# Kernel optimization log

Hardware: AMD Instinct MI355X
Metric: run time of the kernel (lower is better)

The kernel has to match this reference:

```python
import jax, jax.numpy as jnp
import numpy as np

BH = 32  # block_h
BW = 32  # block_w
M, K, N = 4096, 4096, 4096  # tokens, in_features, out_features


def setup_inputs() -> dict:
    key = jax.random.key(0)
    k1, k2, k3, k4 = jax.random.split(key, 4)
    data = jax.random.normal(k1, (M, K), dtype=jnp.float32)
    weight = jax.random.normal(k2, (N, K), dtype=jnp.float32) * 0.02
    bias = jax.random.normal(k3, (N,), dtype=jnp.float32) * 0.02
    # elementwise 0/1 mask over the weight matrix
    mask = jax.random.randint(k4, (N, K), 0, 2, dtype=jnp.int32)
    # conv bias of the 1x1-channel block-summing conv; chosen so ~half the
    # 32x32 blocks (sum ~ Binomial(1024, 0.5)) end up inactive
    conv_bias = jnp.full((1,), -512.0, dtype=jnp.float32)
    return {"data": data, "weight": weight, "bias": bias, "mask": mask,
            "conv_bias": conv_bias}


def reference(data, weight, bias, mask, conv_bias):
    n_out, n_in = weight.shape
    nH, nW = n_out // BH, n_in // BW
    # conv2d with all-ones (BH,BW) kernel, stride (BH,BW) == per-block sum + bias
    block_sum = mask.astype(jnp.float32).reshape(nH, BH, nW, BW).sum(axis=(1, 3))
    block_mask = (block_sum + conv_bias[0]) > 0  # [nH, nW] bool
    # dds matmul (trans_b=True): zero inactive weight blocks, out = data @ W^T
    w_blocks = weight.reshape(nH, BH, nW, BW)
    w_masked = (w_blocks * block_mask[:, None, :, None].astype(weight.dtype)
                ).reshape(n_out, n_in)
    out = jnp.einsum('mk,nk->mn', data, w_masked) + bias
    return out
```

## Files before the change

### kernel.cpp

```cpp
#include <hip/hip_runtime.h>
#include <hip/hip_bf16.h>
#include <stdint.h>

#define M_DIM 4096
#define N_DIM 4096
#define K_DIM 4096
#define NH 128
#define NW 128
#define NKT 64

typedef short bf16x8 __attribute__((ext_vector_type(8)));
typedef short bf16x4 __attribute__((ext_vector_type(4)));
typedef float f32x4 __attribute__((ext_vector_type(4)));

#define MFMA(a, b, c) __builtin_amdgcn_mfma_f32_16x16x32_bf16((a), (b), (c), 0, 0, 0)

__device__ __forceinline__ short f2bf(float f) {
  union { float f; unsigned u; } c; c.f = f;
  unsigned u = c.u;
  unsigned r = (u + 0x7fffu + ((u >> 16) & 1u)) >> 16;
  return (short)r;
}

__global__ __launch_bounds__(256) void k_block_mask(const int* __restrict__ mask,
                                                    const float* __restrict__ conv_bias,
                                                    int* __restrict__ bm) {
  const int bw = blockIdx.x, bh = blockIdx.y;
  const int t = threadIdx.x;
  const int row = t >> 3;
  const int c4 = (t & 7) << 2;
  const int4* p = (const int4*)(mask + (size_t)(bh * 32 + row) * K_DIM + bw * 32 + c4);
  int4 v = *p;
  int s = v.x + v.y + v.z + v.w;
#pragma unroll
  for (int off = 32; off > 0; off >>= 1) s += __shfl_down(s, off);
  __shared__ int red[4];
  if ((t & 63) == 0) red[t >> 6] = s;
  __syncthreads();
  if (t == 0) {
    float tot = (float)(red[0] + red[1] + red[2] + red[3]) + conv_bias[0];
    bm[bh * NW + bw] = (tot > 0.0f) ? 1 : 0;
  }
}

__global__ __launch_bounds__(256) void k_cvt_data(const float* __restrict__ in,
                                                  short* __restrict__ ob) {
  size_t i = (size_t)blockIdx.x * 256 + threadIdx.x;
  f32x4 v = ((const f32x4*)in)[i];
  bf16x4 o;
  o[0] = f2bf(v[0]); o[1] = f2bf(v[1]); o[2] = f2bf(v[2]); o[3] = f2bf(v[3]);
  ((bf16x4*)ob)[i] = o;
}

__global__ __launch_bounds__(256) void k_cvt_weight(const float* __restrict__ w,
                                                    const int* __restrict__ bm,
                                                    short* __restrict__ ob) {
  size_t i = (size_t)blockIdx.x * 256 + threadIdx.x;
  int n = (int)(i >> 10);
  int k = ((int)i & 1023) << 2;
  float m = bm[((n >> 5) << 7) + (k >> 5)] ? 1.0f : 0.0f;
  f32x4 v = ((const f32x4*)w)[i];
  bf16x4 o;
  o[0] = f2bf(v[0] * m); o[1] = f2bf(v[1] * m);
  o[2] = f2bf(v[2] * m); o[3] = f2bf(v[3] * m);
  ((bf16x4*)ob)[i] = o;
}

__global__ __launch_bounds__(512, 2) void k_gemm256(const short* __restrict__ Ab,
                                                    const short* __restrict__ Bb,
                                                    const float* __restrict__ bias,
                                                    const int* __restrict__ bm,
                                                    float* __restrict__ out) {
  __shared__ short Asm[2][2][256][32];
  __shared__ short Bsm[2][2][256][32];

  const int tid = threadIdx.x;
  const int wid = tid >> 6, lane = tid & 63;
  const int r = lane & 15, g0 = lane >> 4;
  const int gs = g0 ^ ((r >> 1) & 3);

  const int swz = (blockIdx.x & 7) * 32 + (blockIdx.x >> 3);
  const int bx = swz & 15, by = swz >> 4;
  const int rowM = by * 256, colN = bx * 256;

  const int srow = tid >> 2;
  const int sseg = (tid & 3) ^ ((tid >> 3) & 3);
  const int swave = wid * 512;

  const short* gA = Ab + (size_t)(rowM + srow) * K_DIM + sseg * 8;
  const short* gB = Bb + (size_t)(colN + srow) * K_DIM + sseg * 8;
  const size_t HOFF = (size_t)128 * K_DIM;

  const int* bp = bm + (size_t)(colN >> 5) * NW;
  unsigned long long m0l = __ballot(bp[0 * 128 + lane] != 0);
  unsigned long long m0h = __ballot(bp[0 * 128 + 64 + lane] != 0);
  unsigned long long m1l = __ballot(bp[1 * 128 + lane] != 0);
  unsigned long long m1h = __ballot(bp[1 * 128 + 64 + lane] != 0);
  unsigned long long m2l = __ballot(bp[2 * 128 + lane] != 0);
  unsigned long long m2h = __ballot(bp[2 * 128 + 64 + lane] != 0);
  unsigned long long m3l = __ballot(bp[3 * 128 + lane] != 0);
  unsigned long long m3h = __ballot(bp[3 * 128 + 64 + lane] != 0);
  unsigned long long m4l = __ballot(bp[4 * 128 + lane] != 0);
  unsigned long long m4h = __ballot(bp[4 * 128 + 64 + lane] != 0);
  unsigned long long m5l = __ballot(bp[5 * 128 + lane] != 0);
  unsigned long long m5h = __ballot(bp[5 * 128 + 64 + lane] != 0);
  unsigned long long m6l = __ballot(bp[6 * 128 + lane] != 0);
  unsigned long long m6h = __ballot(bp[6 * 128 + 64 + lane] != 0);
  unsigned long long m7l = __ballot(bp[7 * 128 + lane] != 0);
  unsigned long long m7h = __ballot(bp[7 * 128 + 64 + lane] != 0);
  __builtin_amdgcn_sched_barrier(0);

#define BTJ(J, kc) ((int)((((kc) & 64) ? m##J##h : m##J##l) >> ((kc) & 63)) & 1)

#define GLL(g, l)                                                            \
  __builtin_amdgcn_global_load_lds((const __attribute__((address_space(1))) void*)(g), \
                                   (__attribute__((address_space(3))) void*)(l), 16, 0, 0)
#define STA(BUF, kt, h, ks) GLL(gA + HOFF * (h) + (size_t)(kt) * 64 + (ks) * 32, \
                                &Asm[BUF][ks][(h) * 128][0] + swave)
#define STB(BUF, kt, h, ks) GLL(gB + HOFF * (h) + (size_t)(kt) * 64 + (ks) * 32, \
                                &Bsm[BUF][ks][(h) * 128][0] + swave)

#define LDA(BUF, ks, m) (*(const bf16x8*)&Asm[BUF][ks][wid * 32 + (m) * 16 + r][gs * 8])
#define LDB(BUF, ks, n) (*(const bf16x8*)&Bsm[BUF][ks][(n) * 16 + r][gs * 8])

#define MFJ(A0, A1, B0, B1, f)                                               \
  acc[0][f] = MFMA(A0, B0, acc[0][f]);   acc[1][f] = MFMA(A1, B0, acc[1][f]); \
  acc[0][(f) + 1] = MFMA(A0, B1, acc[0][(f) + 1]);                           \
  acc[1][(f) + 1] = MFMA(A1, B1, acc[1][(f) + 1]);

#define BAR __builtin_amdgcn_s_barrier()
#define SB0 __builtin_amdgcn_sched_barrier(0)
#define PRIO1 __builtin_amdgcn_s_setprio(1)
#define PRIO0 __builtin_amdgcn_s_setprio(0)
#define VMW_(N) asm volatile("s_waitcnt vmcnt(" #N ")" ::: "memory")
#define VMW(N) VMW_(N)

#define TILE(BUF, NB, u, SB, SA, SR, VM0, VM2)                               \
  {                                                                          \
    const int kb = 2 * (u);                                                  \
    const int c0 = BTJ(0, kb), c1 = BTJ(1, kb), c2 = BTJ(2, kb), c3 = BTJ(3, kb); \
    const int c4 = BTJ(4, kb), c5 = BTJ(5, kb), c6 = BTJ(6, kb), c7 = BTJ(7, kb); \
    const int d0 = BTJ(0, kb + 1), d1 = BTJ(1, kb + 1), d2 = BTJ(2, kb + 1), d3 = BTJ(3, kb + 1); \
    const int d4 = BTJ(4, kb + 1), d5 = BTJ(5, kb + 1), d6 = BTJ(6, kb + 1), d7 = BTJ(7, kb + 1); \
                  \
    BAR; SB0;                                                                \
    aY0 = LDA(BUF, 1, 0); aY1 = LDA(BUF, 1, 1);                              \
    if (c4) { bB[0] = LDB(BUF, 0, 8);  bB[1] = LDB(BUF, 0, 9); }             \
    if (c5) { bB[2] = LDB(BUF, 0, 10); bB[3] = LDB(BUF, 0, 11); }            \
    if (c6) { bB[4] = LDB(BUF, 0, 12); bB[5] = LDB(BUF, 0, 13); }            \
    if (c7) { bB[6] = LDB(BUF, 0, 14); bB[7] = LDB(BUF, 0, 15); }            \
    PRIO1;                                                                   \
    if (c0) { MFJ(aX0, aX1, bA[0], bA[1], 0) }                               \
    if (c1) { MFJ(aX0, aX1, bA[2], bA[3], 2) }                               \
    if (c2) { MFJ(aX0, aX1, bA[4], bA[5], 4) }                               \
    if (c3) { MFJ(aX0, aX1, bA[6], bA[7], 6) }                               \
    PRIO0;                                                                   \
    if (SB) { STB(NB, (u) + 1, 0, 0); STB(NB, (u) + 1, 1, 0); }              \
    VMW(VM0);                                                                \
                          \
    BAR; SB0;                                                                \
    if (d0) { bA[0] = LDB(BUF, 1, 0); bA[1] = LDB(BUF, 1, 1); }              \
    if (d1) { bA[2] = LDB(BUF, 1, 2); bA[3] = LDB(BUF, 1, 3); }              \
    if (d2) { bA[4] = LDB(BUF, 1, 4); bA[5] = LDB(BUF, 1, 5); }              \
    if (d3) { bA[6] = LDB(BUF, 1, 6); bA[7] = LDB(BUF, 1, 7); }              \
    PRIO1;                                                                   \
    if (c4) { MFJ(aX0, aX1, bB[0], bB[1], 8) }                               \
    if (c5) { MFJ(aX0, aX1, bB[2], bB[3], 10) }                              \
    if (c6) { MFJ(aX0, aX1, bB[4], bB[5], 12) }                              \
    if (c7) { MFJ(aX0, aX1, bB[6], bB[7], 14) }                              \
    PRIO0;                                                                   \
    if (SB) { STB(NB, (u) + 1, 0, 1); STB(NB, (u) + 1, 1, 1); }              \
                          \
    BAR; SB0;                                                                \
    if (d4) { bB[0] = LDB(BUF, 1, 8);  bB[1] = LDB(BUF, 1, 9); }             \
    if (d5) { bB[2] = LDB(BUF, 1, 10); bB[3] = LDB(BUF, 1, 11); }            \
    if (d6) { bB[4] = LDB(BUF, 1, 12); bB[5] = LDB(BUF, 1, 13); }            \
    if (d7) { bB[6] = LDB(BUF, 1, 14); bB[7] = LDB(BUF, 1, 15); }            \
    PRIO1;                                                                   \
    if (d0) { MFJ(aY0, aY1, bA[0], bA[1], 0) }                               \
    if (d1) { MFJ(aY0, aY1, bA[2], bA[3], 2) }                               \
    if (d2) { MFJ(aY0, aY1, bA[4], bA[5], 4) }                               \
    if (d3) { MFJ(aY0, aY1, bA[6], bA[7], 6) }                               \
    PRIO0;                                                                   \
    if (SA) { STA(BUF, (u) + 2, 0, 0); STA(BUF, (u) + 2, 1, 0); }            \
    VMW(VM2);                                                                \
       \
    BAR; SB0;                                                                \
    if (SR) {                                                                \
      const int n0 = BTJ(0, kb + 2), n1 = BTJ(1, kb + 2);                    \
      const int n2 = BTJ(2, kb + 2), n3 = BTJ(3, kb + 2);                    \
      aX0 = LDA(NB, 0, 0); aX1 = LDA(NB, 0, 1);                              \
      if (n0) { bA[0] = LDB(NB, 0, 0); bA[1] = LDB(NB, 0, 1); }              \
      if (n1) { bA[2] = LDB(NB, 0, 2); bA[3] = LDB(NB, 0, 3); }              \
      if (n2) { bA[4] = LDB(NB, 0, 4); bA[5] = LDB(NB, 0, 5); }              \
      if (n3) { bA[6] = LDB(NB, 0, 6); bA[7] = LDB(NB, 0, 7); }              \
    }                                                                        \
    PRIO1;                                                                   \
    if (d4) { MFJ(aY0, aY1, bB[0], bB[1], 8) }                               \
    if (d5) { MFJ(aY0, aY1, bB[2], bB[3], 10) }                              \
    if (d6) { MFJ(aY0, aY1, bB[4], bB[5], 12) }                              \
    if (d7) { MFJ(aY0, aY1, bB[6], bB[7], 14) }                              \
    PRIO0;                                                                   \
    if (SA) { STA(BUF, (u) + 2, 0, 1); STA(BUF, (u) + 2, 1, 1); }            \
  }

  f32x4 acc[2][16];
#pragma unroll
  for (int m = 0; m < 2; ++m)
#pragma unroll
    for (int n = 0; n < 16; ++n) acc[m][n] = (f32x4){0.f, 0.f, 0.f, 0.f};

  bf16x8 aX0, aX1, aY0, aY1, bA[8], bB[8];

  STA(0, 0, 0, 0); STA(0, 0, 1, 0); STA(0, 0, 0, 1); STA(0, 0, 1, 1);
  STB(0, 0, 0, 0); STB(0, 0, 1, 0); STB(0, 0, 0, 1); STB(0, 0, 1, 1);
  STA(1, 1, 0, 0); STA(1, 1, 1, 0); STA(1, 1, 0, 1); STA(1, 1, 1, 1);
  VMW(4);
  BAR; SB0;
  {
    const int p0 = BTJ(0, 0), p1 = BTJ(1, 0), p2 = BTJ(2, 0), p3 = BTJ(3, 0);
    aX0 = LDA(0, 0, 0); aX1 = LDA(0, 0, 1);
    if (p0) { bA[0] = LDB(0, 0, 0); bA[1] = LDB(0, 0, 1); }
    if (p1) { bA[2] = LDB(0, 0, 2); bA[3] = LDB(0, 0, 3); }
    if (p2) { bA[4] = LDB(0, 0, 4); bA[5] = LDB(0, 0, 5); }
    if (p3) { bA[6] = LDB(0, 0, 6); bA[7] = LDB(0, 0, 7); }
  }

#pragma unroll 1
  for (int u = 0; u < NKT - 2; u += 2) {
    TILE(0, 1, u, 1, 1, 1, 6, 4);
    TILE(1, 0, u + 1, 1, 1, 1, 6, 4);
  }
  TILE(0, 1, NKT - 2, 1, 0, 1, 6, 2);
  TILE(1, 0, NKT - 1, 0, 0, 0, 0, 0);

  const int orow = rowM + wid * 32;
#pragma unroll
  for (int n = 0; n < 16; ++n) {
    int col = colN + n * 16 + r;
    float bz = bias[col];
#pragma unroll
    for (int m = 0; m < 2; ++m) {
      int row0 = orow + m * 16 + g0 * 4;
#pragma unroll
      for (int j = 0; j < 4; ++j)
        out[(size_t)(row0 + j) * N_DIM + col] = acc[m][n][j] + bz;
    }
  }
#undef TILE
#undef GLL
#undef STA
#undef STB
#undef LDA
#undef LDB
#undef MFJ
#undef BAR
#undef SB0
#undef PRIO1
#undef PRIO0
#undef VMW
#undef VMW_
#undef BTJ
}

__global__ __launch_bounds__(256) void k_naive(const float* __restrict__ A,
                                               const float* __restrict__ W,
                                               const float* __restrict__ bias,
                                               const int* __restrict__ bm,
                                               float* __restrict__ out) {
  int col = blockIdx.x * 16 + (threadIdx.x & 15);
  int row = blockIdx.y * 16 + (threadIdx.x >> 4);
  float s = 0.f;
  for (int kb = 0; kb < K_DIM / 32; ++kb) {
    if (bm[(col >> 5) * NW + kb]) {
      int kbase = kb * 32;
#pragma unroll 8
      for (int k = 0; k < 32; ++k)
        s += A[(size_t)row * K_DIM + kbase + k] * W[(size_t)col * K_DIM + kbase + k];
    }
  }
  out[(size_t)row * N_DIM + col] = s + bias[col];
}

extern "C" void kernel_launch(void* const* d_in, const int* in_sizes, int n_in,
                              void* d_out, int out_size, void* d_ws, size_t ws_size,
                              hipStream_t stream) {
  const float* data = (const float*)d_in[0];
  const float* weight = (const float*)d_in[1];
  const float* bias = (const float*)d_in[2];
  const int* mask = (const int*)d_in[3];
  const float* conv_bias = (const float*)d_in[4];
  float* out = (float*)d_out;

  int* bm = (int*)d_ws;
  const size_t off_a = 65536;
  const size_t off_b = off_a + (size_t)M_DIM * K_DIM * 2;
  const size_t needed = off_b + (size_t)N_DIM * K_DIM * 2;

  k_block_mask<<<dim3(NW, NH), 256, 0, stream>>>(mask, conv_bias, bm);

  if (ws_size >= needed) {
    short* Abf = (short*)((char*)d_ws + off_a);
    short* Wbf = (short*)((char*)d_ws + off_b);
    k_cvt_data<<<dim3((M_DIM * (K_DIM / 4)) / 256), 256, 0, stream>>>(data, Abf);
    k_cvt_weight<<<dim3((N_DIM * (K_DIM / 4)) / 256), 256, 0, stream>>>(weight, bm, Wbf);
    k_gemm256<<<dim3(256), 512, 0, stream>>>(Abf, Wbf, bias, bm, out);
  } else {
    k_naive<<<dim3(N_DIM / 16, M_DIM / 16), 256, 0, stream>>>(data, weight, bias, bm, out);
  }
}
```

Measured before the change: 152.4 us.

## Replace fine-grained 4-barrier pipeline with single-barrier double buffer per tile

Restructures the main loop from a finely interleaved schedule (four barriers per tile, staggered A/B global-to-LDS loads with partial vmcnt waits, prefetch of next tile's fragments) to a simple double buffer. All next-tile global loads are issued at the start of each tile, and a full vmcnt(0) wait plus one barrier sits at the end. It also skips A-fragment LDS reads when a half-tile has no active blocks. This cuts barrier count and simplifies the code, but loses the fine overlap of LDS reads with MFMAs and waits for all loads each tile.

```diff
diff --git a/kernel.cpp b/kernel.cpp
--- a/kernel.cpp
+++ b/kernel.cpp
@@ -132,76 +132,72 @@
 #define SB0 __builtin_amdgcn_sched_barrier(0)
 #define PRIO1 __builtin_amdgcn_s_setprio(1)
 #define PRIO0 __builtin_amdgcn_s_setprio(0)
-#define VMW_(N) asm volatile("s_waitcnt vmcnt(" #N ")" ::: "memory")
-#define VMW(N) VMW_(N)
-
-#define TILE(BUF, NB, u, SB, SA, SR, VM0, VM2)                               \
+#define VMW0 asm volatile("s_waitcnt vmcnt(0)" ::: "memory")
+
+#define TILE(BUF, NB, u, SG)                                                 \
   {                                                                          \
     const int kb = 2 * (u);                                                  \
     const int c0 = BTJ(0, kb), c1 = BTJ(1, kb), c2 = BTJ(2, kb), c3 = BTJ(3, kb); \
     const int c4 = BTJ(4, kb), c5 = BTJ(5, kb), c6 = BTJ(6, kb), c7 = BTJ(7, kb); \
     const int d0 = BTJ(0, kb + 1), d1 = BTJ(1, kb + 1), d2 = BTJ(2, kb + 1), d3 = BTJ(3, kb + 1); \
     const int d4 = BTJ(4, kb + 1), d5 = BTJ(5, kb + 1), d6 = BTJ(6, kb + 1), d7 = BTJ(7, kb + 1); \
-                  \
-    BAR; SB0;                                                                \
-    aY0 = LDA(BUF, 1, 0); aY1 = LDA(BUF, 1, 1);                              \
+    const int anyC = c0 | c1 | c2 | c3 | c4 | c5 | c6 | c7;                  \
+    const int anyD = d0 | d1 | d2 | d3 | d4 | d5 | d6 | d7;                  \
+    if (SG) {                                                                \
+      STA(NB, (u) + 1, 0, 0); STA(NB, (u) + 1, 1, 0);                        \
+      STA(NB, (u) + 1, 0, 1); STA(NB, (u) + 1, 1, 1);                        \
+      STB(NB, (u) + 1, 0, 0); STB(NB, (u) + 1, 1, 0);                        \
+      STB(NB, (u) + 1, 0, 1); STB(NB, (u) + 1, 1, 1);                        \
+    }                                                                        \
+                                                 \
+    if (anyC) { aX0 = LDA(BUF, 0, 0); aX1 = LDA(BUF, 0, 1); }                \
+    if (c0) { bA[0] = LDB(BUF, 0, 0); bA[1] = LDB(BUF, 0, 1); }              \
+    if (c1) { bA[2] = LDB(BUF, 0, 2); bA[3] = LDB(BUF, 0, 3); }              \
+    if (c2) { bA[4] = LDB(BUF, 0, 4); bA[5] = LDB(BUF, 0, 5); }              \
+    if (c3) { bA[6] = LDB(BUF, 0, 6); bA[7] = LDB(BUF, 0, 7); }              \
+                                                         \
     if (c4) { bB[0] = LDB(BUF, 0, 8);  bB[1] = LDB(BUF, 0, 9); }             \
     if (c5) { bB[2] = LDB(BUF, 0, 10); bB[3] = LDB(BUF, 0, 11); }            \
     if (c6) { bB[4] = LDB(BUF, 0, 12); bB[5] = LDB(BUF, 0, 13); }            \
     if (c7) { bB[6] = LDB(BUF, 0, 14); bB[7] = LDB(BUF, 0, 15); }            \
+                                                           \
     PRIO1;                                                                   \
     if (c0) { MFJ(aX0, aX1, bA[0], bA[1], 0) }                               \
     if (c1) { MFJ(aX0, aX1, bA[2], bA[3], 2) }                               \
     if (c2) { MFJ(aX0, aX1, bA[4], bA[5], 4) }                               \
     if (c3) { MFJ(aX0, aX1, bA[6], bA[7], 6) }                               \
     PRIO0;                                                                   \
-    if (SB) { STB(NB, (u) + 1, 0, 0); STB(NB, (u) + 1, 1, 0); }              \
-    VMW(VM0);                                                                \
-                          \
-    BAR; SB0;                                                                \
+                                                 \
+    if (anyD) { aY0 = LDA(BUF, 1, 0); aY1 = LDA(BUF, 1, 1); }                \
     if (d0) { bA[0] = LDB(BUF, 1, 0); bA[1] = LDB(BUF, 1, 1); }              \
     if (d1) { bA[2] = LDB(BUF, 1, 2); bA[3] = LDB(BUF, 1, 3); }              \
     if (d2) { bA[4] = LDB(BUF, 1, 4); bA[5] = LDB(BUF, 1, 5); }              \
     if (d3) { bA[6] = LDB(BUF, 1, 6); bA[7] = LDB(BUF, 1, 7); }              \
+                                                           \
     PRIO1;                                                                   \
     if (c4) { MFJ(aX0, aX1, bB[0], bB[1], 8) }                               \
     if (c5) { MFJ(aX0, aX1, bB[2], bB[3], 10) }                              \
     if (c6) { MFJ(aX0, aX1, bB[4], bB[5], 12) }                              \
     if (c7) { MFJ(aX0, aX1, bB[6], bB[7], 14) }                              \
     PRIO0;                                                                   \
-    if (SB) { STB(NB, (u) + 1, 0, 1); STB(NB, (u) + 1, 1, 1); }              \
-                          \
-    BAR; SB0;                                                                \
+                                                         \
     if (d4) { bB[0] = LDB(BUF, 1, 8);  bB[1] = LDB(BUF, 1, 9); }             \
     if (d5) { bB[2] = LDB(BUF, 1, 10); bB[3] = LDB(BUF, 1, 11); }            \
     if (d6) { bB[4] = LDB(BUF, 1, 12); bB[5] = LDB(BUF, 1, 13); }            \
     if (d7) { bB[6] = LDB(BUF, 1, 14); bB[7] = LDB(BUF, 1, 15); }            \
+                                                           \
     PRIO1;                                                                   \
     if (d0) { MFJ(aY0, aY1, bA[0], bA[1], 0) }                               \
     if (d1) { MFJ(aY0, aY1, bA[2], bA[3], 2) }                               \
     if (d2) { MFJ(aY0, aY1, bA[4], bA[5], 4) }                               \
     if (d3) { MFJ(aY0, aY1, bA[6], bA[7], 6) }                               \
-    PRIO0;                                                                   \
-    if (SA) { STA(BUF, (u) + 2, 0, 0); STA(BUF, (u) + 2, 1, 0); }            \
-    VMW(VM2);                                                                \
-       \
-    BAR; SB0;                                                                \
-    if (SR) {                                                                \
-      const int n0 = BTJ(0, kb + 2), n1 = BTJ(1, kb + 2);                    \
-      const int n2 = BTJ(2, kb + 2), n3 = BTJ(3, kb + 2);                    \
-      aX0 = LDA(NB, 0, 0); aX1 = LDA(NB, 0, 1);                              \
-      if (n0) { bA[0] = LDB(NB, 0, 0); bA[1] = LDB(NB, 0, 1); }              \
-      if (n1) { bA[2] = LDB(NB, 0, 2); bA[3] = LDB(NB, 0, 3); }              \
-      if (n2) { bA[4] = LDB(NB, 0, 4); bA[5] = LDB(NB, 0, 5); }              \
-      if (n3) { bA[6] = LDB(NB, 0, 6); bA[7] = LDB(NB, 0, 7); }              \
-    }                                                                        \
-    PRIO1;                                                                   \
+                                                           \
     if (d4) { MFJ(aY0, aY1, bB[0], bB[1], 8) }                               \
     if (d5) { MFJ(aY0, aY1, bB[2], bB[3], 10) }                              \
     if (d6) { MFJ(aY0, aY1, bB[4], bB[5], 12) }                              \
     if (d7) { MFJ(aY0, aY1, bB[6], bB[7], 14) }                              \
     PRIO0;                                                                   \
-    if (SA) { STA(BUF, (u) + 2, 0, 1); STA(BUF, (u) + 2, 1, 1); }            \
+    VMW0; BAR; SB0;                                                          \
   }
 
   f32x4 acc[2][16];
@@ -214,25 +210,16 @@
 
   STA(0, 0, 0, 0); STA(0, 0, 1, 0); STA(0, 0, 0, 1); STA(0, 0, 1, 1);
   STB(0, 0, 0, 0); STB(0, 0, 1, 0); STB(0, 0, 0, 1); STB(0, 0, 1, 1);
-  STA(1, 1, 0, 0); STA(1, 1, 1, 0); STA(1, 1, 0, 1); STA(1, 1, 1, 1);
-  VMW(4);
+  VMW0;
   BAR; SB0;
-  {
-    const int p0 = BTJ(0, 0), p1 = BTJ(1, 0), p2 = BTJ(2, 0), p3 = BTJ(3, 0);
-    aX0 = LDA(0, 0, 0); aX1 = LDA(0, 0, 1);
-    if (p0) { bA[0] = LDB(0, 0, 0); bA[1] = LDB(0, 0, 1); }
-    if (p1) { bA[2] = LDB(0, 0, 2); bA[3] = LDB(0, 0, 3); }
-    if (p2) { bA[4] = LDB(0, 0, 4); bA[5] = LDB(0, 0, 5); }
-    if (p3) { bA[6] = LDB(0, 0, 6); bA[7] = LDB(0, 0, 7); }
-  }
 
 #pragma unroll 1
   for (int u = 0; u < NKT - 2; u += 2) {
-    TILE(0, 1, u, 1, 1, 1, 6, 4);
-    TILE(1, 0, u + 1, 1, 1, 1, 6, 4);
-  }
-  TILE(0, 1, NKT - 2, 1, 0, 1, 6, 2);
-  TILE(1, 0, NKT - 1, 0, 0, 0, 0, 0);
+    TILE(0, 1, u, 1);
+    TILE(1, 0, u + 1, 1);
+  }
+  TILE(0, 1, NKT - 2, 1);
+  TILE(1, 0, NKT - 1, 0);
 
   const int orow = rowM + wid * 32;
 #pragma unroll
@@ -258,8 +245,7 @@
 #undef SB0
 #undef PRIO1
 #undef PRIO0
-#undef VMW
-#undef VMW_
+#undef VMW0
 #undef BTJ
 }
 
```

After: 177.0 us. +16.1%, slower.
